# Optimization experiments

Hardware: AMD Instinct MI355X
Metric: run time of the kernel (lower is better)

Reference implementation:

```python
import jax, jax.numpy as jnp
import numpy as np


def setup_inputs() -> dict:
    key = jax.random.key(0)
    kx, kw = jax.random.split(key)
    x = jax.random.normal(kx, (4, 2048, 4096), dtype=jnp.float32)
    weight = jax.random.normal(kw, (4096, 4096), dtype=jnp.float32) * 0.02
    return {"x": x, "weight": weight}


def _binact(x):
    """BiReal piecewise sign approximation with STE: forward = sign(x),
    backward flows through the clipped quadratic surrogate out3."""
    m1 = x < -1.0
    m2 = x < 0.0
    m3 = x < 1.0
    out1 = jnp.where(m1, -1.0, x * x + 2.0 * x)
    out2 = jnp.where(m2, out1, -x * x + 2.0 * x)
    out3 = jnp.where(m3, out2, 1.0)
    return jax.lax.stop_gradient(jnp.sign(x) - out3) + out3


def _quant_weight(w):
    """Per-output-row mean-abs scale * sign(w), STE through clamp(w,-1,1)."""
    scale = jax.lax.stop_gradient(jnp.mean(jnp.abs(w), axis=1, keepdims=True))
    bw_no_grad = scale * jnp.sign(w)  # [out, in]
    clipped = jnp.clip(w, -1.0, 1.0)
    return jax.lax.stop_gradient(bw_no_grad - clipped) + clipped


def reference(x, weight):
    xq = _binact(x)               # [B, S, in]
    wq = _quant_weight(weight)    # [out, in]
    # F.linear(input, w) with no bias: x @ w.T
    return jnp.einsum('bsi,oi->bso', xq, wq)
```

## Files before the change

kernel.cpp:

```cpp
#include <hip/hip_runtime.h>
#include <stdint.h>

typedef unsigned short u16;
typedef __attribute__((ext_vector_type(4))) int i32x4;

#define BM 128
#define BN 128
#define BKB 64

__device__ __forceinline__ uint32_t sign_i8(float v) {
  return v > 0.f ? 1u : (v < 0.f ? 0xFFu : 0u);
}

__device__ __forceinline__ uint32_t pack4(float a, float b, float c, float d) {
  return sign_i8(a) | (sign_i8(b) << 8) | (sign_i8(c) << 16) | (sign_i8(d) << 24);
}

__global__ void quant_x_kernel(const float4* __restrict__ x, int4* __restrict__ xq, int n16) {
  int i = blockIdx.x * 256 + threadIdx.x;
  if (i >= n16) return;
  float4 v0 = x[i * 4 + 0], v1 = x[i * 4 + 1], v2 = x[i * 4 + 2], v3 = x[i * 4 + 3];
  int4 s;
  s.x = (int)pack4(v0.x, v0.y, v0.z, v0.w);
  s.y = (int)pack4(v1.x, v1.y, v1.z, v1.w);
  s.z = (int)pack4(v2.x, v2.y, v2.z, v2.w);
  s.w = (int)pack4(v3.x, v3.y, v3.z, v3.w);
  xq[i] = s;
}

__global__ void quant_w_kernel(const float* __restrict__ w, uint8_t* __restrict__ wq,
                               float* __restrict__ scale, int K) {
  const int row = blockIdx.x;
  const int t = threadIdx.x;
  const float* wr = w + (size_t)row * K;
  uint8_t* wqr = wq + (size_t)row * K;
  float asum = 0.f;
  for (int p = 0; p < K; p += 1024) {
    int idx = p + t * 4;
    float4 v = *(const float4*)(wr + idx);
    uint32_t s = pack4(v.x, v.y, v.z, v.w);
    *(uint32_t*)(wqr + idx) = s;
    asum += fabsf(v.x) + fabsf(v.y) + fabsf(v.z) + fabsf(v.w);
  }
  __shared__ float red[256];
  red[t] = asum;
  __syncthreads();
  for (int s2 = 128; s2 > 0; s2 >>= 1) {
    if (t < s2) red[t] += red[t + s2];
    __syncthreads();
  }
  if (t == 0) scale[row] = red[0] / (float)K;
}

__device__ __forceinline__ void load16(const uint8_t* g, uint8_t* l) {
  __builtin_amdgcn_global_load_lds(
      (const __attribute__((address_space(1))) uint32_t*)(uintptr_t)g,
      (__attribute__((address_space(3))) uint32_t*)(uintptr_t)l,
      16, 0, 0);
}

__global__ __launch_bounds__(256, 3) void gemm_bt_kernel(
    const uint8_t* __restrict__ A, const uint8_t* __restrict__ B,
    const float* __restrict__ scale, float* __restrict__ C,
    int M, int N, int K) {
  __shared__ __align__(16) uint8_t As[BM * BKB];
  __shared__ __align__(16) uint8_t Bs[BN * BKB];

  const int tid = threadIdx.x;
  const int lane = tid & 63;
  const int wave = tid >> 6;
  const int waveM = wave & 1;
  const int waveN = wave >> 1;

  const int rowA0 = blockIdx.y * BM;
  const int rowB0 = blockIdx.x * BN;

  const uint8_t* aG = A + (size_t)(rowA0 + wave * 32 + (lane >> 2)) * K + (lane & 3) * 16;
  const uint8_t* bG = B + (size_t)(rowB0 + wave * 32 + (lane >> 2)) * K + (lane & 3) * 16;
  uint8_t* aL = As + wave * 2048 + lane * 16;
  uint8_t* bL = Bs + wave * 2048 + lane * 16;
  const size_t stride16 = (size_t)16 * K;

  const int fRow = lane & 15;
  const int fKB = (lane >> 4) * 16;
  const uint8_t* aF = As + (waveM * 64 + fRow) * BKB + fKB;
  const uint8_t* bF = Bs + (waveN * 64 + fRow) * BKB + fKB;

  i32x4 acc[4][4] = {};

  for (int k0 = 0; k0 < K; k0 += BKB) {
    __syncthreads();
    load16(aG + k0, aL);
    load16(aG + k0 + stride16, aL + 1024);
    load16(bG + k0, bL);
    load16(bG + k0 + stride16, bL + 1024);
    __syncthreads();

    i32x4 av[4], bv[4];
#pragma unroll
    for (int i = 0; i < 4; ++i) {
      av[i] = *(const i32x4*)(aF + i * 16 * BKB);
      bv[i] = *(const i32x4*)(bF + i * 16 * BKB);
    }
#pragma unroll
    for (int mi = 0; mi < 4; ++mi)
#pragma unroll
      for (int ni = 0; ni < 4; ++ni)
        acc[mi][ni] =
            __builtin_amdgcn_mfma_i32_16x16x64_i8(av[mi], bv[ni], acc[mi][ni], 0, 0, 0);
  }

  const int cRow0 = rowA0 + waveM * 64 + ((lane >> 4) * 4);
  const int cCol0 = rowB0 + waveN * 64 + (lane & 15);
  float sc[4];
#pragma unroll
  for (int ni = 0; ni < 4; ++ni) sc[ni] = scale[cCol0 + ni * 16];
#pragma unroll
  for (int mi = 0; mi < 4; ++mi)
#pragma unroll
    for (int ni = 0; ni < 4; ++ni)
#pragma unroll
      for (int r = 0; r < 4; ++r)
        C[(size_t)(cRow0 + mi * 16 + r) * N + (cCol0 + ni * 16)] =
            (float)acc[mi][ni][r] * sc[ni];
}

__global__ void fallback_gemm(const float* __restrict__ X, const float* __restrict__ W,
                              float* __restrict__ C, int M, int N, int K) {
  __shared__ float xs[16][65];
  __shared__ float ws[16][65];
  __shared__ float wabs[256];
  __shared__ float scl[16];
  const int tx = threadIdx.x, ty = threadIdx.y;
  const int t = ty * 16 + tx;
  float acc = 0.f, wa = 0.f;
  for (int k0 = 0; k0 < K; k0 += 64) {
    __syncthreads();
#pragma unroll
    for (int j = 0; j < 4; ++j) {
      int e = t * 4 + j;
      int r = e >> 6, c = e & 63;
      float xv = X[(size_t)(blockIdx.y * 16 + r) * K + k0 + c];
      xs[r][c] = xv > 0.f ? 1.f : (xv < 0.f ? -1.f : 0.f);
      float wv = W[(size_t)(blockIdx.x * 16 + r) * K + k0 + c];
      ws[r][c] = wv > 0.f ? 1.f : (wv < 0.f ? -1.f : 0.f);
      wa += fabsf(wv);
    }
    __syncthreads();
#pragma unroll 8
    for (int k = 0; k < 64; ++k) acc += xs[ty][k] * ws[tx][k];
  }
  wabs[t] = wa;
  __syncthreads();
  for (int s2 = 8; s2 > 0; s2 >>= 1) {
    if (tx < s2) wabs[t] += wabs[t + s2];
    __syncthreads();
  }
  if (tx == 0) scl[ty] = wabs[t] / (float)K;
  __syncthreads();
  C[(size_t)(blockIdx.y * 16 + ty) * N + (blockIdx.x * 16 + tx)] = acc * scl[tx];
}

extern "C" void kernel_launch(void* const* d_in, const int* in_sizes, int n_in,
                              void* d_out, int out_size, void* d_ws, size_t ws_size,
                              hipStream_t stream) {
  const float* x = (const float*)d_in[0];
  const float* w = (const float*)d_in[1];
  float* out = (float*)d_out;

  const int K = 4096;
  const int N = in_sizes[1] / K;
  const int M = in_sizes[0] / K;

  size_t need = (size_t)M * K + (size_t)N * K + (size_t)N * sizeof(float);
  if (ws_size >= need) {
    uint8_t* Xq = (uint8_t*)d_ws;
    uint8_t* Wq = Xq + (size_t)M * K;
    float* scale = (float*)(Wq + (size_t)N * K);

    int n16 = (M * K) / 16;
    quant_x_kernel<<<(n16 + 255) / 256, 256, 0, stream>>>((const float4*)x, (int4*)Xq, n16);
    quant_w_kernel<<<N, 256, 0, stream>>>(w, Wq, scale, K);

    dim3 grid(N / BN, M / BM);
    gemm_bt_kernel<<<grid, 256, 0, stream>>>(Xq, Wq, scale, out, M, N, K);
  } else {
    dim3 grid(N / 16, M / 16);
    fallback_gemm<<<grid, dim3(16, 16), 0, stream>>>(x, w, out, M, N, K);
  }
}
```

Before: 402.5 us.

## Quantize signs to FP4 nibbles and use scaled 32x32x64 f8f6f4 MFMA

Packs the sign values of x and weight as 4-bit FP4 (E2M1) codes (+1 = 0x2, -1 = 0xA) instead of int8. This halves quantized storage and the bytes the GEMM loads per K step. The GEMM now uses mfma_scale_f32_32x32x64_f8f6f4 with FP4 operands and unit scales, on 32x32 tiles, so each 64-byte LDS tile covers 128 K values and the K-loop has half the iterations. The risks are the unusual 32x32 output layout mapping and correctness of the operand packing, where only half of each i32x8 register is filled.

New measurement: 342.9 us. -14.8%, faster.

```diff
diff --git a/kernel.cpp b/kernel.cpp
--- a/kernel.cpp
+++ b/kernel.cpp
@@ -1,30 +1,32 @@
 #include <hip/hip_runtime.h>
 #include <stdint.h>
 
-typedef unsigned short u16;
 typedef __attribute__((ext_vector_type(4))) int i32x4;
+typedef __attribute__((ext_vector_type(8))) int i32x8;
+typedef __attribute__((ext_vector_type(16))) float f32x16;
 
 #define BM 128
 #define BN 128
-#define BKB 64
-
-__device__ __forceinline__ uint32_t sign_i8(float v) {
-  return v > 0.f ? 1u : (v < 0.f ? 0xFFu : 0u);
-}
-
-__device__ __forceinline__ uint32_t pack4(float a, float b, float c, float d) {
-  return sign_i8(a) | (sign_i8(b) << 8) | (sign_i8(c) << 16) | (sign_i8(d) << 24);
-}
-
-__global__ void quant_x_kernel(const float4* __restrict__ x, int4* __restrict__ xq, int n16) {
+
+__device__ __forceinline__ uint32_t nib4(float v) {
+  return v > 0.f ? 0x2u : (v < 0.f ? 0xAu : 0u);
+}
+
+__device__ __forceinline__ uint32_t pack8(float4 a, float4 b) {
+  return nib4(a.x) | (nib4(a.y) << 4) | (nib4(a.z) << 8) | (nib4(a.w) << 12) |
+         (nib4(b.x) << 16) | (nib4(b.y) << 20) | (nib4(b.z) << 24) | (nib4(b.w) << 28);
+}
+
+__global__ void quant_x_kernel(const float4* __restrict__ x, int4* __restrict__ xq, int n) {
   int i = blockIdx.x * 256 + threadIdx.x;
-  if (i >= n16) return;
-  float4 v0 = x[i * 4 + 0], v1 = x[i * 4 + 1], v2 = x[i * 4 + 2], v3 = x[i * 4 + 3];
+  if (i >= n) return;
+  float4 v0 = x[i * 8 + 0], v1 = x[i * 8 + 1], v2 = x[i * 8 + 2], v3 = x[i * 8 + 3];
+  float4 v4 = x[i * 8 + 4], v5 = x[i * 8 + 5], v6 = x[i * 8 + 6], v7 = x[i * 8 + 7];
   int4 s;
-  s.x = (int)pack4(v0.x, v0.y, v0.z, v0.w);
-  s.y = (int)pack4(v1.x, v1.y, v1.z, v1.w);
-  s.z = (int)pack4(v2.x, v2.y, v2.z, v2.w);
-  s.w = (int)pack4(v3.x, v3.y, v3.z, v3.w);
+  s.x = (int)pack8(v0, v1);
+  s.y = (int)pack8(v2, v3);
+  s.z = (int)pack8(v4, v5);
+  s.w = (int)pack8(v6, v7);
   xq[i] = s;
 }
 
@@ -32,16 +34,16 @@
                                float* __restrict__ scale, int K) {
   const int row = blockIdx.x;
   const int t = threadIdx.x;
-  const float* wr = w + (size_t)row * K;
-  uint8_t* wqr = wq + (size_t)row * K;
-  float asum = 0.f;
-  for (int p = 0; p < K; p += 1024) {
-    int idx = p + t * 4;
-    float4 v = *(const float4*)(wr + idx);
-    uint32_t s = pack4(v.x, v.y, v.z, v.w);
-    *(uint32_t*)(wqr + idx) = s;
-    asum += fabsf(v.x) + fabsf(v.y) + fabsf(v.z) + fabsf(v.w);
-  }
+  const float4* wr4 = (const float4*)(w + (size_t)row * K);
+  float4 v0 = wr4[t * 4 + 0], v1 = wr4[t * 4 + 1], v2 = wr4[t * 4 + 2], v3 = wr4[t * 4 + 3];
+  uint2 o;
+  o.x = pack8(v0, v1);
+  o.y = pack8(v2, v3);
+  ((uint2*)(wq + (size_t)row * (K / 2)))[t] = o;
+  float asum = fabsf(v0.x) + fabsf(v0.y) + fabsf(v0.z) + fabsf(v0.w) +
+               fabsf(v1.x) + fabsf(v1.y) + fabsf(v1.z) + fabsf(v1.w) +
+               fabsf(v2.x) + fabsf(v2.y) + fabsf(v2.z) + fabsf(v2.w) +
+               fabsf(v3.x) + fabsf(v3.y) + fabsf(v3.z) + fabsf(v3.w);
   __shared__ float red[256];
   red[t] = asum;
   __syncthreads();
@@ -63,8 +65,8 @@
     const uint8_t* __restrict__ A, const uint8_t* __restrict__ B,
     const float* __restrict__ scale, float* __restrict__ C,
     int M, int N, int K) {
-  __shared__ __align__(16) uint8_t As[BM * BKB];
-  __shared__ __align__(16) uint8_t Bs[BN * BKB];
+  __shared__ __align__(16) uint8_t As[BM * 64];
+  __shared__ __align__(16) uint8_t Bs[BN * 64];
 
   const int tid = threadIdx.x;
   const int lane = tid & 63;
@@ -75,54 +77,65 @@
   const int rowA0 = blockIdx.y * BM;
   const int rowB0 = blockIdx.x * BN;
 
-  const uint8_t* aG = A + (size_t)(rowA0 + wave * 32 + (lane >> 2)) * K + (lane & 3) * 16;
-  const uint8_t* bG = B + (size_t)(rowB0 + wave * 32 + (lane >> 2)) * K + (lane & 3) * 16;
+  const int KB = K / 2;
+
+  const uint8_t* aG = A + (size_t)(rowA0 + wave * 32 + (lane >> 2)) * KB + (lane & 3) * 16;
+  const uint8_t* bG = B + (size_t)(rowB0 + wave * 32 + (lane >> 2)) * KB + (lane & 3) * 16;
   uint8_t* aL = As + wave * 2048 + lane * 16;
   uint8_t* bL = Bs + wave * 2048 + lane * 16;
-  const size_t stride16 = (size_t)16 * K;
-
-  const int fRow = lane & 15;
-  const int fKB = (lane >> 4) * 16;
-  const uint8_t* aF = As + (waveM * 64 + fRow) * BKB + fKB;
-  const uint8_t* bF = Bs + (waveN * 64 + fRow) * BKB + fKB;
-
-  i32x4 acc[4][4] = {};
-
-  for (int k0 = 0; k0 < K; k0 += BKB) {
-    __syncthreads();
-    load16(aG + k0, aL);
-    load16(aG + k0 + stride16, aL + 1024);
-    load16(bG + k0, bL);
-    load16(bG + k0 + stride16, bL + 1024);
-    __syncthreads();
-
-    i32x4 av[4], bv[4];
-#pragma unroll
-    for (int i = 0; i < 4; ++i) {
-      av[i] = *(const i32x4*)(aF + i * 16 * BKB);
-      bv[i] = *(const i32x4*)(bF + i * 16 * BKB);
+  const size_t strideG16 = (size_t)16 * KB;
+
+  const uint8_t* aF = As + (size_t)(waveM * 64 + (lane & 31)) * 64 + (lane >> 5) * 16;
+  const uint8_t* bF = Bs + (size_t)(waveN * 64 + (lane & 31)) * 64 + (lane >> 5) * 16;
+
+  f32x16 acc[2][2] = {};
+  i32x8 aop[2] = {}, bop[2] = {};
+
+  for (int kb = 0; kb < KB; kb += 64) {
+    __syncthreads();
+    load16(aG + kb, aL);
+    load16(aG + kb + strideG16, aL + 1024);
+    load16(bG + kb, bL);
+    load16(bG + kb + strideG16, bL + 1024);
+    __syncthreads();
+
+#pragma unroll
+    for (int s = 0; s < 2; ++s) {
+#pragma unroll
+      for (int mi = 0; mi < 2; ++mi) {
+        i32x4 t = *(const i32x4*)(aF + mi * 32 * 64 + s * 32);
+        aop[mi].s0 = t.x; aop[mi].s1 = t.y; aop[mi].s2 = t.z; aop[mi].s3 = t.w;
+      }
+#pragma unroll
+      for (int ni = 0; ni < 2; ++ni) {
+        i32x4 t = *(const i32x4*)(bF + ni * 32 * 64 + s * 32);
+        bop[ni].s0 = t.x; bop[ni].s1 = t.y; bop[ni].s2 = t.z; bop[ni].s3 = t.w;
+      }
+#pragma unroll
+      for (int mi = 0; mi < 2; ++mi)
+#pragma unroll
+        for (int ni = 0; ni < 2; ++ni)
+          acc[mi][ni] = __builtin_amdgcn_mfma_scale_f32_32x32x64_f8f6f4(
+              aop[mi], bop[ni], acc[mi][ni],
+               4,  4,
+               0, 0x7f7f7f7f,  0, 0x7f7f7f7f);
     }
-#pragma unroll
-    for (int mi = 0; mi < 4; ++mi)
-#pragma unroll
-      for (int ni = 0; ni < 4; ++ni)
-        acc[mi][ni] =
-            __builtin_amdgcn_mfma_i32_16x16x64_i8(av[mi], bv[ni], acc[mi][ni], 0, 0, 0);
-  }
-
-  const int cRow0 = rowA0 + waveM * 64 + ((lane >> 4) * 4);
-  const int cCol0 = rowB0 + waveN * 64 + (lane & 15);
-  float sc[4];
-#pragma unroll
-  for (int ni = 0; ni < 4; ++ni) sc[ni] = scale[cCol0 + ni * 16];
-#pragma unroll
-  for (int mi = 0; mi < 4; ++mi)
-#pragma unroll
-    for (int ni = 0; ni < 4; ++ni)
-#pragma unroll
-      for (int r = 0; r < 4; ++r)
-        C[(size_t)(cRow0 + mi * 16 + r) * N + (cCol0 + ni * 16)] =
-            (float)acc[mi][ni][r] * sc[ni];
+  }
+
+  const int cCol = rowB0 + waveN * 64 + (lane & 31);
+  const int cRowBase = rowA0 + waveM * 64 + 4 * (lane >> 5);
+  float sc[2];
+#pragma unroll
+  for (int ni = 0; ni < 2; ++ni) sc[ni] = scale[cCol + ni * 32];
+#pragma unroll
+  for (int mi = 0; mi < 2; ++mi)
+#pragma unroll
+    for (int ni = 0; ni < 2; ++ni)
+#pragma unroll
+      for (int r = 0; r < 16; ++r) {
+        int row = cRowBase + mi * 32 + (r & 3) + 8 * (r >> 2);
+        C[(size_t)row * N + cCol + ni * 32] = acc[mi][ni][r] * sc[ni];
+      }
 }
 
 __global__ void fallback_gemm(const float* __restrict__ X, const float* __restrict__ W,
@@ -172,14 +185,14 @@
   const int N = in_sizes[1] / K;
   const int M = in_sizes[0] / K;
 
-  size_t need = (size_t)M * K + (size_t)N * K + (size_t)N * sizeof(float);
+  size_t need = (size_t)M * (K / 2) + (size_t)N * (K / 2) + (size_t)N * sizeof(float);
   if (ws_size >= need) {
     uint8_t* Xq = (uint8_t*)d_ws;
-    uint8_t* Wq = Xq + (size_t)M * K;
-    float* scale = (float*)(Wq + (size_t)N * K);
-
-    int n16 = (M * K) / 16;
-    quant_x_kernel<<<(n16 + 255) / 256, 256, 0, stream>>>((const float4*)x, (int4*)Xq, n16);
+    uint8_t* Wq = Xq + (size_t)M * (K / 2);
+    float* scale = (float*)(Wq + (size_t)N * (K / 2));
+
+    int n32 = (M * K) / 32;
+    quant_x_kernel<<<(n32 + 255) / 256, 256, 0, stream>>>((const float4*)x, (int4*)Xq, n32);
     quant_w_kernel<<<N, 256, 0, stream>>>(w, Wq, scale, K);
 
     dim3 grid(N / BN, M / BM);
```
